# Optimization experiments

Measured on AMD Instinct MI355X. Metric: run time of the kernel, lower is better.

## Reference

```python
import jax, jax.numpy as jnp
import numpy as np

N = 8192          # number of nodes
IN_F = 256        # in_features
OUT_F = 128       # out_features
ALPHA = 0.2       # LeakyReLU negative slope


def setup_inputs() -> dict:
    key = jax.random.key(0)
    k1, k2, k3, k4 = jax.random.split(key, 4)
    h = jax.random.normal(k1, (N, IN_F), dtype=jnp.float32)
    adj = jax.random.randint(k2, (N, N), 0, 2, dtype=jnp.int32)  # dense 0/1 adjacency mask
    W = (jax.random.normal(k3, (IN_F, OUT_F), dtype=jnp.float32) * 0.05)   # W.weight^T
    a = (jax.random.normal(k4, (2 * OUT_F,), dtype=jnp.float32) * 0.05)    # a.weight flattened
    return {"h": h, "adj": adj, "W": W, "a": a}


def reference(h, adj, W, a):
    # Wh = self.W(h): [N, OUT_F]
    Wh = h @ W
    # Original builds an [N, N, 2F] concat tensor then projects with 'a'.
    # Equivalent math: e[i, j] = leaky_relu(Wh[i]@a1 + Wh[j]@a2)
    a1, a2 = a[:OUT_F], a[OUT_F:]
    src = Wh @ a1                                     # [N] per-source score
    dst = Wh @ a2                                     # [N] per-target score
    e = jax.nn.leaky_relu(src[:, None] + dst[None, :], negative_slope=ALPHA)  # [N, N]
    # masked softmax over neighbors (dim=1); adj==0 -> -inf
    e = jnp.where(adj == 0, -jnp.inf, e)
    attention = jax.nn.softmax(e, axis=1)             # [N, N]
    # dropout p=0 in eval-mode reference -> identity
    h_prime = attention @ Wh                          # [N, OUT_F]
    return jax.nn.elu(h_prime)                        # concat=True -> ELU
```

## Files before the change

kernel.cpp:

```cpp
#include <hip/hip_runtime.h>
#include <math.h>

#define N 8192
#define IN_F 256
#define OUT_F 128
#define ALPHA 0.2f
#define JS 8
#define NSTEP 32
#define MW (N / 32)

typedef _Float16 f16;
typedef __attribute__((ext_vector_type(4))) float f32x4;
typedef __attribute__((ext_vector_type(8))) _Float16 f16x8;
typedef __attribute__((ext_vector_type(4))) _Float16 f16x4;

__global__ __launch_bounds__(256) void k_prep(const float* __restrict__ W,
                                              f16* __restrict__ WT) {
    int idx = blockIdx.x * 256 + threadIdx.x;
    int f = idx >> 8;
    int k = idx & 255;
    WT[idx] = (f16)W[k * OUT_F + f];
}

__global__ __launch_bounds__(256) void k_pack(const int* __restrict__ adj,
                                              unsigned* __restrict__ M) {
    const int t = threadIdx.x;
    const int l = t & 63;
    const size_t tot = (size_t)N * N / 4;
    const size_t stride = (size_t)gridDim.x * 256;
    size_t idx = (size_t)blockIdx.x * 256 + t;
    const int4* ap = (const int4*)adj;
    for (; idx < tot; idx += stride) {
        int4 v = ap[idx];
        unsigned m = (v.x ? 1u : 0u) | (v.y ? 2u : 0u) | (v.z ? 4u : 0u) | (v.w ? 8u : 0u);
        m |= __shfl_down(m, 1) << 4;
        m |= __shfl_down(m, 2) << 8;
        m |= __shfl_down(m, 4) << 16;
        if ((l & 7) == 0) M[idx >> 3] = m;
    }
}

#define HS 280
__global__ __launch_bounds__(256) void k_wh(const float* __restrict__ h,
                                            const f16* __restrict__ WT,
                                            const float* __restrict__ a,
                                            f16* __restrict__ Bpack,
                                            float* __restrict__ src,
                                            float* __restrict__ dst) {
    __shared__ __align__(16) f16 hA[32][HS];
    __shared__ __align__(16) f16 outT[128][40];
    __shared__ float sred[4][32], dred[4][32];

    const int t = threadIdx.x;
    const int i0 = blockIdx.x * 32;
    const int wv = t >> 6, l = t & 63, ln = l & 15, lq = l >> 4;

    {
        const float4* hg = (const float4*)(h + (size_t)i0 * IN_F);
#pragma unroll
        for (int it = 0; it < 8; ++it) {
            int idx = t + it * 256;
            int r = idx >> 6;
            int c4 = (idx & 63) * 4;
            float4 v = hg[idx];
            f16x4 p = { (f16)v.x, (f16)v.y, (f16)v.z, (f16)v.w };
            *(f16x4*)&hA[r][c4] = p;
        }
    }
    __syncthreads();

    f32x4 acc00 = {0.f,0.f,0.f,0.f}, acc01 = {0.f,0.f,0.f,0.f};
    f32x4 acc10 = {0.f,0.f,0.f,0.f}, acc11 = {0.f,0.f,0.f,0.f};
    const int f0 = 32 * wv;

#pragma unroll
    for (int ks = 0; ks < 8; ++ks) {
        const int k0 = 32 * ks + 8 * lq;
        f16x8 a0 = *(const f16x8*)&hA[ln][k0];
        f16x8 a1 = *(const f16x8*)&hA[16 + ln][k0];
        f16x8 b0 = *(const f16x8*)(WT + (size_t)(f0 + ln) * IN_F + k0);
        f16x8 b1 = *(const f16x8*)(WT + (size_t)(f0 + 16 + ln) * IN_F + k0);
        acc00 = __builtin_amdgcn_mfma_f32_16x16x32_f16(a0, b0, acc00, 0, 0, 0);
        acc01 = __builtin_amdgcn_mfma_f32_16x16x32_f16(a0, b1, acc01, 0, 0, 0);
        acc10 = __builtin_amdgcn_mfma_f32_16x16x32_f16(a1, b0, acc10, 0, 0, 0);
        acc11 = __builtin_amdgcn_mfma_f32_16x16x32_f16(a1, b1, acc11, 0, 0, 0);
    }

    const float a1c0 = a[f0 + ln],      a2c0 = a[128 + f0 + ln];
    const float a1c1 = a[f0 + 16 + ln], a2c1 = a[128 + f0 + 16 + ln];
    float sp[8], dp[8];
#pragma unroll
    for (int i = 0; i < 8; ++i) { sp[i] = 0.f; dp[i] = 0.f; }

#pragma unroll
    for (int hh = 0; hh < 2; ++hh) {
        f32x4 v0 = hh ? acc10 : acc00;
        f32x4 v1 = hh ? acc11 : acc01;
        f16x4 p0, p1;
#pragma unroll
        for (int rg = 0; rg < 4; ++rg) {
            sp[hh * 4 + rg] += v0[rg] * a1c0 + v1[rg] * a1c1;
            dp[hh * 4 + rg] += v0[rg] * a2c0 + v1[rg] * a2c1;
            p0[rg] = (f16)v0[rg];
            p1[rg] = (f16)v1[rg];
        }
        *(f16x4*)&outT[f0 + ln][16 * hh + 4 * lq] = p0;
        *(f16x4*)&outT[f0 + 16 + ln][16 * hh + 4 * lq] = p1;
    }
#pragma unroll
    for (int i = 0; i < 8; ++i) {
        float s = sp[i], d = dp[i];
        s += __shfl_down(s, 8, 16); d += __shfl_down(d, 8, 16);
        s += __shfl_down(s, 4, 16); d += __shfl_down(d, 4, 16);
        s += __shfl_down(s, 2, 16); d += __shfl_down(d, 2, 16);
        s += __shfl_down(s, 1, 16); d += __shfl_down(d, 1, 16);
        if (ln == 0) {
            int row = 16 * (i >> 2) + 4 * lq + (i & 3);
            sred[wv][row] = s;
            dred[wv][row] = d;
        }
    }
    __syncthreads();
    if (t < 32) {
        src[i0 + t] = sred[0][t] + sred[1][t] + sred[2][t] + sred[3][t];
        dst[i0 + t] = dred[0][t] + dred[1][t] + dred[2][t] + dred[3][t];
    }
    {
        const size_t gs = (size_t)(i0 >> 5);
        const int ft0 = t >> 6;
#pragma unroll
        for (int hh = 0; hh < 2; ++hh) {
            const int ft = ft0 + 4 * hh;
            f16x8 v = *(const f16x8*)&outT[16 * ft + ln][8 * lq];
            *(f16x8*)(Bpack + (gs * 8 + ft) * 512 + l * 8) = v;
        }
    }
}

__global__ __launch_bounds__(256, 1) void k_attn(const unsigned* __restrict__ M,
                                                 const f16* __restrict__ Bpack,
                                                 const float* __restrict__ src,
                                                 const float* __restrict__ dst,
                                                 float* __restrict__ p_part,
                                                 float* __restrict__ l_part) {
    const int t = threadIdx.x;
    const int wv = t >> 6, l = t & 63, ln = l & 15, lq = l >> 4;
    const int i0 = (blockIdx.x * 4 + wv) * 32;
    const int jq = blockIdx.y;

    const float src0 = src[i0 + ln];
    const float src1 = src[i0 + 16 + ln];
    const float c0 = fabsf(src0) + 4.0f;
    const float c1 = fabsf(src1) + 4.0f;
    float lp0 = 0.f, lp1 = 0.f;

    f32x4 acc0[8], acc1[8];
#pragma unroll
    for (int ft = 0; ft < 8; ++ft) {
        acc0[ft] = (f32x4){0.f,0.f,0.f,0.f};
        acc1[ft] = (f32x4){0.f,0.f,0.f,0.f};
    }

    const unsigned* Mr0 = M + (size_t)(i0 + ln) * MW + jq * NSTEP;
    const unsigned* Mr1 = Mr0 + (size_t)16 * MW;
    const float* drow = dst + jq * (N / JS) + 8 * lq;
    const f16* Bb = Bpack + (size_t)(jq * NSTEP) * 8 * 512 + l * 8;

    uint4 m0c = *(const uint4*)Mr0;
    uint4 m1c = *(const uint4*)Mr1;
    float4 cd0 = *(const float4*)(drow);
    float4 cd1 = *(const float4*)(drow + 4);

    for (int g = 0; g < 8; ++g) {
        uint4 m0n, m1n;
        if (g < 7) {
            m0n = *(const uint4*)(Mr0 + 4 * (g + 1));
            m1n = *(const uint4*)(Mr1 + 4 * (g + 1));
        }
#pragma unroll
        for (int s4 = 0; s4 < 4; ++s4) {
            const int s = 4 * g + s4;
            const f16* bp = Bb + (size_t)s * (8 * 512);
            f16x8 bf[8];
#pragma unroll
            for (int ft = 0; ft < 8; ++ft)
                bf[ft] = *(const f16x8*)(bp + ft * 512);
            const float4 d0 = cd0, d1 = cd1;
            {
                const int off = 32 * ((s + 1) & (NSTEP - 1));
                cd0 = *(const float4*)(drow + off);
                cd1 = *(const float4*)(drow + off + 4);
            }
            const unsigned b0 = (((const unsigned*)&m0c)[s4] >> (8 * lq)) & 0xffu;
            const unsigned b1 = (((const unsigned*)&m1c)[s4] >> (8 * lq)) & 0xffu;
            const float* df0 = (const float*)&d0;
            const float* df1 = (const float*)&d1;
            f16x8 af0, af1;
#pragma unroll
            for (int k = 0; k < 8; ++k) {
                const float dv = (k < 4) ? df0[k] : df1[k - 4];
                float e0 = src0 + dv;
                float w0 = (b0 >> k) & 1u ? __expf(fmaxf(e0, ALPHA * e0) - c0) : 0.f;
                lp0 += w0; af0[k] = (f16)w0;
                float e1 = src1 + dv;
                float w1 = (b1 >> k) & 1u ? __expf(fmaxf(e1, ALPHA * e1) - c1) : 0.f;
                lp1 += w1; af1[k] = (f16)w1;
            }
#pragma unroll
            for (int ft = 0; ft < 8; ++ft) {
                acc0[ft] = __builtin_amdgcn_mfma_f32_16x16x32_f16(af0, bf[ft], acc0[ft], 0, 0, 0);
                acc1[ft] = __builtin_amdgcn_mfma_f32_16x16x32_f16(af1, bf[ft], acc1[ft], 0, 0, 0);
            }
        }
        if (g < 7) { m0c = m0n; m1c = m1n; }
    }

    lp0 += __shfl_down(lp0, 32); lp0 += __shfl_down(lp0, 16);
    lp1 += __shfl_down(lp1, 32); lp1 += __shfl_down(lp1, 16);
    if (l < 16) {
        l_part[(size_t)jq * N + i0 + l] = lp0;
        l_part[(size_t)jq * N + i0 + 16 + l] = lp1;
    }

    float* pb = p_part + (size_t)jq * N * OUT_F;
#pragma unroll
    for (int ft = 0; ft < 8; ++ft) {
#pragma unroll
        for (int rg = 0; rg < 4; ++rg) {
            pb[(size_t)(i0 + 4 * lq + rg) * OUT_F + 16 * ft + ln] = acc0[ft][rg];
            pb[(size_t)(i0 + 16 + 4 * lq + rg) * OUT_F + 16 * ft + ln] = acc1[ft][rg];
        }
    }
}

__global__ __launch_bounds__(256) void k_comb(const float* __restrict__ p_part,
                                              const float* __restrict__ l_part,
                                              float* __restrict__ out) {
    const int idx4 = blockIdx.x * 256 + threadIdx.x;
    const int row = idx4 >> 5;
    const float4* pp = (const float4*)p_part;
    float4 p = pp[idx4];
    float lsum = l_part[row];
#pragma unroll
    for (int q = 1; q < JS; ++q) {
        float4 v = pp[(size_t)q * (N * OUT_F / 4) + idx4];
        p.x += v.x; p.y += v.y; p.z += v.z; p.w += v.w;
        lsum += l_part[(size_t)q * N + row];
    }
    float inv = 1.0f / lsum;
    float4 r;
    r.x = p.x * inv; r.x = r.x > 0.f ? r.x : expm1f(r.x);
    r.y = p.y * inv; r.y = r.y > 0.f ? r.y : expm1f(r.y);
    r.z = p.z * inv; r.z = r.z > 0.f ? r.z : expm1f(r.z);
    r.w = p.w * inv; r.w = r.w > 0.f ? r.w : expm1f(r.w);
    ((float4*)out)[idx4] = r;
}

extern "C" void kernel_launch(void* const* d_in, const int* in_sizes, int n_in,
                              void* d_out, int out_size, void* d_ws, size_t ws_size,
                              hipStream_t stream) {
    const float* h   = (const float*)d_in[0];
    const int*   adj = (const int*)d_in[1];
    const float* W   = (const float*)d_in[2];
    const float* a   = (const float*)d_in[3];
    float* out = (float*)d_out;

    char* ws = (char*)d_ws;
    f16*      WT     = (f16*)ws;        ws += 64 * 1024;
    f16*      Bpack  = (f16*)ws;        ws += 2 * 1024 * 1024;
    float*    src    = (float*)ws;      ws += N * sizeof(float);
    float*    dst    = (float*)ws;      ws += N * sizeof(float);
    float*    l_part = (float*)ws;      ws += (size_t)JS * N * sizeof(float);
    unsigned* M      = (unsigned*)ws;   ws += (size_t)N * MW * sizeof(unsigned);
    float*    p_part = (float*)ws;

    k_pack<<<2048, 256, 0, stream>>>(adj, M);
    k_prep<<<128, 256, 0, stream>>>(W, WT);
    k_wh<<<N / 32, 256, 0, stream>>>(h, WT, a, Bpack, src, dst);
    dim3 agrid(N / 128, JS);
    k_attn<<<agrid, 256, 0, stream>>>(M, Bpack, src, dst, p_part, l_part);
    k_comb<<<N * OUT_F / 4 / 256, 256, 0, stream>>>(p_part, l_part, out);
}
```

Before: 419.0 us.

## Halve rows per wave in attention kernel to raise occupancy

Each wave of the attention kernel now handles 16 rows instead of 32, so it keeps one accumulator set instead of two. The launch bound moves from 1 to 4 blocks per CU and the grid doubles. The aim is to cut register pressure and hide memory and exp latency with more resident waves. In exchange, each B fragment loaded from Bpack now feeds one MFMA instead of two, which doubles B-operand global traffic, and the B loads are no longer issued ahead of the softmax math.

```diff
diff --git a/kernel.cpp b/kernel.cpp
--- a/kernel.cpp
+++ b/kernel.cpp
@@ -137,7 +137,7 @@
     }
 }
 
-__global__ __launch_bounds__(256, 1) void k_attn(const unsigned* __restrict__ M,
+__global__ __launch_bounds__(256, 4) void k_attn(const unsigned* __restrict__ M,
                                                  const f16* __restrict__ Bpack,
                                                  const float* __restrict__ src,
                                                  const float* __restrict__ dst,
@@ -145,90 +145,68 @@
                                                  float* __restrict__ l_part) {
     const int t = threadIdx.x;
     const int wv = t >> 6, l = t & 63, ln = l & 15, lq = l >> 4;
-    const int i0 = (blockIdx.x * 4 + wv) * 32;
+    const int i0 = (blockIdx.x * 4 + wv) * 16;
     const int jq = blockIdx.y;
 
     const float src0 = src[i0 + ln];
-    const float src1 = src[i0 + 16 + ln];
     const float c0 = fabsf(src0) + 4.0f;
-    const float c1 = fabsf(src1) + 4.0f;
-    float lp0 = 0.f, lp1 = 0.f;
-
-    f32x4 acc0[8], acc1[8];
-#pragma unroll
-    for (int ft = 0; ft < 8; ++ft) {
-        acc0[ft] = (f32x4){0.f,0.f,0.f,0.f};
-        acc1[ft] = (f32x4){0.f,0.f,0.f,0.f};
-    }
+    float lp0 = 0.f;
+
+    f32x4 acc[8];
+#pragma unroll
+    for (int ft = 0; ft < 8; ++ft) acc[ft] = (f32x4){0.f,0.f,0.f,0.f};
 
     const unsigned* Mr0 = M + (size_t)(i0 + ln) * MW + jq * NSTEP;
-    const unsigned* Mr1 = Mr0 + (size_t)16 * MW;
     const float* drow = dst + jq * (N / JS) + 8 * lq;
     const f16* Bb = Bpack + (size_t)(jq * NSTEP) * 8 * 512 + l * 8;
 
-    uint4 m0c = *(const uint4*)Mr0;
-    uint4 m1c = *(const uint4*)Mr1;
+    uint4 mc = *(const uint4*)Mr0;
     float4 cd0 = *(const float4*)(drow);
     float4 cd1 = *(const float4*)(drow + 4);
 
     for (int g = 0; g < 8; ++g) {
-        uint4 m0n, m1n;
-        if (g < 7) {
-            m0n = *(const uint4*)(Mr0 + 4 * (g + 1));
-            m1n = *(const uint4*)(Mr1 + 4 * (g + 1));
-        }
+        uint4 mn;
+        if (g < 7) mn = *(const uint4*)(Mr0 + 4 * (g + 1));
 #pragma unroll
         for (int s4 = 0; s4 < 4; ++s4) {
             const int s = 4 * g + s4;
-            const f16* bp = Bb + (size_t)s * (8 * 512);
-            f16x8 bf[8];
-#pragma unroll
-            for (int ft = 0; ft < 8; ++ft)
-                bf[ft] = *(const f16x8*)(bp + ft * 512);
             const float4 d0 = cd0, d1 = cd1;
             {
                 const int off = 32 * ((s + 1) & (NSTEP - 1));
                 cd0 = *(const float4*)(drow + off);
                 cd1 = *(const float4*)(drow + off + 4);
             }
-            const unsigned b0 = (((const unsigned*)&m0c)[s4] >> (8 * lq)) & 0xffu;
-            const unsigned b1 = (((const unsigned*)&m1c)[s4] >> (8 * lq)) & 0xffu;
+            const unsigned b0 = (((const unsigned*)&mc)[s4] >> (8 * lq)) & 0xffu;
             const float* df0 = (const float*)&d0;
             const float* df1 = (const float*)&d1;
-            f16x8 af0, af1;
+            f16x8 af;
 #pragma unroll
             for (int k = 0; k < 8; ++k) {
                 const float dv = (k < 4) ? df0[k] : df1[k - 4];
                 float e0 = src0 + dv;
                 float w0 = (b0 >> k) & 1u ? __expf(fmaxf(e0, ALPHA * e0) - c0) : 0.f;
-                lp0 += w0; af0[k] = (f16)w0;
-                float e1 = src1 + dv;
-                float w1 = (b1 >> k) & 1u ? __expf(fmaxf(e1, ALPHA * e1) - c1) : 0.f;
-                lp1 += w1; af1[k] = (f16)w1;
+                lp0 += w0; af[k] = (f16)w0;
             }
+            const f16* bp = Bb + (size_t)s * (8 * 512);
 #pragma unroll
             for (int ft = 0; ft < 8; ++ft) {
-                acc0[ft] = __builtin_amdgcn_mfma_f32_16x16x32_f16(af0, bf[ft], acc0[ft], 0, 0, 0);
-                acc1[ft] = __builtin_amdgcn_mfma_f32_16x16x32_f16(af1, bf[ft], acc1[ft], 0, 0, 0);
+                f16x8 bf = *(const f16x8*)(bp + ft * 512);
+                acc[ft] = __builtin_amdgcn_mfma_f32_16x16x32_f16(af, bf, acc[ft], 0, 0, 0);
             }
         }
-        if (g < 7) { m0c = m0n; m1c = m1n; }
-    }
-
-    lp0 += __shfl_down(lp0, 32); lp0 += __shfl_down(lp0, 16);
-    lp1 += __shfl_down(lp1, 32); lp1 += __shfl_down(lp1, 16);
-    if (l < 16) {
-        l_part[(size_t)jq * N + i0 + l] = lp0;
-        l_part[(size_t)jq * N + i0 + 16 + l] = lp1;
-    }
+        if (g < 7) mc = mn;
+    }
+
+    lp0 += __shfl_down(lp0, 32);
+    lp0 += __shfl_down(lp0, 16);
+    if (l < 16) l_part[(size_t)jq * N + i0 + l] = lp0;
 
     float* pb = p_part + (size_t)jq * N * OUT_F;
 #pragma unroll
     for (int ft = 0; ft < 8; ++ft) {
 #pragma unroll
         for (int rg = 0; rg < 4; ++rg) {
-            pb[(size_t)(i0 + 4 * lq + rg) * OUT_F + 16 * ft + ln] = acc0[ft][rg];
-            pb[(size_t)(i0 + 16 + 4 * lq + rg) * OUT_F + 16 * ft + ln] = acc1[ft][rg];
+            pb[(size_t)(i0 + 4 * lq + rg) * OUT_F + 16 * ft + ln] = acc[ft][rg];
         }
     }
 }
@@ -277,7 +255,7 @@
     k_pack<<<2048, 256, 0, stream>>>(adj, M);
     k_prep<<<128, 256, 0, stream>>>(W, WT);
     k_wh<<<N / 32, 256, 0, stream>>>(h, WT, a, Bpack, src, dst);
-    dim3 agrid(N / 128, JS);
+    dim3 agrid(N / 64, JS);
     k_attn<<<agrid, 256, 0, stream>>>(M, Bpack, src, dst, p_part, l_part);
     k_comb<<<N * OUT_F / 4 / 256, 256, 0, stream>>>(p_part, l_part, out);
 }
```

Measured after the change: 429.8 us. +2.6%, slower.
